# Kernel tuning notes

Hardware: AMD Instinct MI355X
Metric: run time of the kernel (lower is better)

Reference implementation:

```python
import jax, jax.numpy as jnp
import numpy as np

N_NODES = 200_000
N_UND = 3_200_000        # undirected masked edges
E = 2 * N_UND            # directed edges


def _seg_mean(m, dst, n_nodes):
    # DGL fn.mean: mean over incoming edge messages; zero-in-degree nodes get 0.
    s = jax.ops.segment_sum(m, dst, num_segments=n_nodes)
    deg = jax.ops.segment_sum(jnp.ones((m.shape[0], 1), m.dtype), dst, num_segments=n_nodes)
    return s / jnp.maximum(deg, 1.0)


def setup_inputs() -> dict:
    key = jax.random.key(0)
    ks = jax.random.split(key, 18)
    w = lambda k, s: jax.random.normal(k, s, dtype=jnp.float32) * 0.1
    return {
        'node_feat': jax.random.normal(ks[0], (N_NODES, 7), dtype=jnp.float32),
        'edge_feat': jax.random.normal(ks[1], (E, 4), dtype=jnp.float32),
        'edge_mask': jax.random.normal(ks[2], (N_UND, 1), dtype=jnp.float32),
        'src': jax.random.randint(ks[3], (E,), 0, N_NODES),
        'dst': jax.random.randint(ks[4], (E,), 0, N_NODES),
        'W1a': w(ks[5], (11, 32)), 'b1a': jnp.zeros((32,), jnp.float32),
        'W1b': w(ks[6], (32, 32)), 'b1b': jnp.zeros((32,), jnp.float32),
        'W2a': w(ks[7], (32, 32)), 'b2a': jnp.zeros((32,), jnp.float32),
        'W2b': w(ks[8], (32, 32)), 'b2b': jnp.zeros((32,), jnp.float32),
        'Wm1': w(ks[9], (32, 16)), 'bm1': jnp.zeros((16,), jnp.float32),
        'Wm2': w(ks[10], (16, 2)), 'bm2': jnp.zeros((2,), jnp.float32),
    }


def reference(node_feat, edge_feat, edge_mask, src, dst,
              W1a, b1a, W1b, b1b, W2a, b2a, W2b, b2b, Wm1, bm1, Wm2, bm2):
    n_nodes = node_feat.shape[0]
    relu = jax.nn.relu
    # interleave mask to both edge directions: [m0, m0, m1, m1, ...]
    m_full = jax.nn.sigmoid(jnp.repeat(edge_mask, 2, axis=0))  # [E, 1]
    # layer 1: masked cat(edge_h, src_h) -> mean over dst -> MLP
    msg1 = m_full * jnp.concatenate([edge_feat, node_feat[src]], axis=1)  # [E, 11]
    h = _seg_mean(msg1, dst, n_nodes)                                      # [N, 11]
    h = relu(relu(h @ W1a + b1a) @ W1b + b1b)                              # [N, 32]
    # layer 2: masked src_h -> mean over dst -> MLP
    msg2 = m_full * h[src]                                                 # [E, 32]
    h = _seg_mean(msg2, dst, n_nodes)                                      # [N, 32]
    h = relu(relu(h @ W2a + b2a) @ W2b + b2b)                              # [N, 32]
    # global max pool + readout MLP + softmax (batch_size=1 path)
    g = jnp.max(h, axis=0)                                                 # [32]
    logits = relu(g @ Wm1 + bm1) @ Wm2 + bm2                               # [2]
    return jax.nn.softmax(logits)[None, :]                                 # [1, 2]
```

## Files before the change

kernel.cpp:

```cpp
#include <hip/hip_runtime.h>
#include <hip/hip_fp16.h>
#include <math.h>

#define SCHUNK 1024
#define PMAX   80
#define BSHIFT 9
#define MAXBKT 1024
#define BINB   1024
#define EPT    8

__device__ __forceinline__ float sigmoidf_(float x) {
    return 1.0f / (1.0f + __expf(-x));
}

union I2H { int i; __half2 h; };
__device__ __forceinline__ int pack_h2(float a, float b) {
    I2H u; u.h = __floats2half2_rn(a, b); return u.i;
}
__device__ __forceinline__ float2 unpack_h2(int w) {
    I2H u; u.i = w; return __half22float2(u.h);
}

typedef int v4i_nt __attribute__((ext_vector_type(4)));
typedef float v4f_nt __attribute__((ext_vector_type(4)));
__device__ __forceinline__ int4 ldnt16(const int4* p) {
    v4i_nt v = __builtin_nontemporal_load((const v4i_nt*)p);
    return make_int4(v[0], v[1], v[2], v[3]);
}
__device__ __forceinline__ float4 ldnt16f(const float* p) {
    v4f_nt v = __builtin_nontemporal_load((const v4f_nt*)p);
    return make_float4(v[0], v[1], v[2], v[3]);
}

__global__ void hist_rank(const int* __restrict__ dst, int* __restrict__ deg,
                          int* __restrict__ rank, int E) {
    int e = blockIdx.x * blockDim.x + threadIdx.x;
    if (e < E) rank[e] = atomicAdd(&deg[dst[e]], 1);
}

__global__ void scan_part(const int* __restrict__ deg, int* __restrict__ bsum, int N) {
    __shared__ int tot[256];
    int t = threadIdx.x;
    int base = blockIdx.x * SCHUNK + t * 4;
    int s = 0;
    if (base + 3 < N) {
        int4 v = *(const int4*)(deg + base);
        s = v.x + v.y + v.z + v.w;
    } else {
#pragma unroll
        for (int j = 0; j < 4; ++j) if (base + j < N) s += deg[base + j];
    }
    tot[t] = s;
    __syncthreads();
    for (int o = 128; o >= 1; o >>= 1) {
        if (t < o) tot[t] += tot[t + o];
        __syncthreads();
    }
    if (t == 0) bsum[blockIdx.x] = tot[0];
}

__global__ void scan_mid(int* __restrict__ bsum, int* __restrict__ off, int B, int N) {
    __shared__ int tmp[256];
    int t = threadIdx.x;
    int chunk = (B + 255) / 256;
    int lo = t * chunk, hi = min(lo + chunk, B);
    int s = 0;
    for (int i = lo; i < hi; ++i) s += bsum[i];
    tmp[t] = s;
    __syncthreads();
    for (int o = 1; o < 256; o <<= 1) {
        int v = (t >= o) ? tmp[t - o] : 0;
        __syncthreads();
        tmp[t] += v;
        __syncthreads();
    }
    int run = (t == 0) ? 0 : tmp[t - 1];
    for (int i = lo; i < hi; ++i) { int d = bsum[i]; bsum[i] = run; run += d; }
    if (t == 255) off[N] = tmp[255];
}

__global__ void scan_fin(const int* __restrict__ deg, const int* __restrict__ bsum,
                         int* __restrict__ off, int N) {
    __shared__ int tots[256];
    int t = threadIdx.x;
    int base = blockIdx.x * SCHUNK + t * 4;
    int v0 = 0, v1 = 0, v2 = 0, v3 = 0;
    if (base + 3 < N) {
        int4 v = *(const int4*)(deg + base);
        v0 = v.x; v1 = v.y; v2 = v.z; v3 = v.w;
    } else {
        if (base + 0 < N) v0 = deg[base + 0];
        if (base + 1 < N) v1 = deg[base + 1];
        if (base + 2 < N) v2 = deg[base + 2];
        if (base + 3 < N) v3 = deg[base + 3];
    }
    tots[t] = v0 + v1 + v2 + v3;
    __syncthreads();
    for (int o = 1; o < 256; o <<= 1) {
        int v = (t >= o) ? tots[t - o] : 0;
        __syncthreads();
        tots[t] += v;
        __syncthreads();
    }
    int run = bsum[blockIdx.x] + ((t == 0) ? 0 : tots[t - 1]);
    if (base + 0 < N) off[base + 0] = run; run += v0;
    if (base + 1 < N) off[base + 1] = run; run += v1;
    if (base + 2 < N) off[base + 2] = run; run += v2;
    if (base + 3 < N) off[base + 3] = run;
}

__global__ void pack_nodes(const float* __restrict__ nf, int4* __restrict__ nf16, int N) {
    int n = blockIdx.x * blockDim.x + threadIdx.x;
    if (n >= N) return;
    const float* p = nf + (size_t)n * 7;
    int4 w;
    w.x = pack_h2(p[0], p[1]);
    w.y = pack_h2(p[2], p[3]);
    w.z = pack_h2(p[4], p[5]);
    w.w = pack_h2(p[6], 0.0f);
    nf16[n] = w;
}

__global__ __launch_bounds__(BINB)
void binA(const int* __restrict__ dst, const int* __restrict__ src,
          const float* __restrict__ edge_mask, const float* __restrict__ edge_feat,
          const float* __restrict__ node_feat,
          int* __restrict__ bktCnt, int4* __restrict__ region, int4* __restrict__ nf16,
          int E, int N, int nbkt, int bcap) {
    __shared__ int cnt[MAXBKT];
    __shared__ int base[MAXBKT];
    int t = threadIdx.x;
    int gt = blockIdx.x * BINB + t;
    if (gt < N) {
        const float* p = node_feat + (size_t)gt * 7;
        int4 w;
        w.x = pack_h2(p[0], p[1]);
        w.y = pack_h2(p[2], p[3]);
        w.z = pack_h2(p[4], p[5]);
        w.w = pack_h2(p[6], 0.0f);
        nf16[gt] = w;
    }
    for (int i = t; i < nbkt; i += BINB) cnt[i] = 0;
    __syncthreads();
    int4 rec[EPT];
    int  bl[EPT];
    int e0 = blockIdx.x * (BINB * EPT) + t;
#pragma unroll
    for (int j = 0; j < EPT; ++j) {
        int e = e0 + j * BINB;
        bl[j] = -1;
        if (e < E) {
            int d = dst[e];
            int s = src[e];
            float m = sigmoidf_(edge_mask[e >> 1]);
            float4 ef = ldnt16f(edge_feat + (size_t)e * 4);
            int b = d >> BSHIFT;
            int dlo = d & ((1 << BSHIFT) - 1);
            int lr = atomicAdd(&cnt[b], 1);
            rec[j].x = (dlo << 18) | s;
            rec[j].y = pack_h2(m * ef.x, m * ef.y);
            rec[j].z = pack_h2(m * ef.z, m * ef.w);
            rec[j].w = __float_as_int(m);
            bl[j] = (b << 16) | lr;
        }
    }
    __syncthreads();
    for (int i = t; i < nbkt; i += BINB)
        base[i] = atomicAdd(&bktCnt[i], cnt[i]);
    __syncthreads();
#pragma unroll
    for (int j = 0; j < EPT; ++j) {
        if (bl[j] >= 0) {
            int b = bl[j] >> 16, lr = bl[j] & 0xffff;
            int pos = base[b] + lr;
            if (pos < bcap) region[(size_t)b * bcap + pos] = rec[j];
        }
    }
}

__global__ __launch_bounds__(1024)
void fillS(const int4* __restrict__ region, const int* __restrict__ bktCnt,
           int4* __restrict__ recP, int* __restrict__ deg, int N, int bcap) {
    __shared__ int cnt[1 << BSHIFT];
    int b = blockIdx.x;
    int t = threadIdx.x;
    if (t < (1 << BSHIFT)) cnt[t] = 0;
    __syncthreads();
    int count = min(bktCnt[b], bcap);
    const int4* reg = region + (size_t)b * bcap;
    int n0 = b << BSHIFT;
    for (int i = t; i < count; i += blockDim.x) {
        int4 w = ldnt16(reg + i);
        int dlo = ((unsigned)w.x) >> 18;
        int r = atomicAdd(&cnt[dlo], 1);
        if (r < PMAX) {
            w.x &= 0x3FFFF;
            recP[(size_t)(n0 + dlo) * PMAX + r] = w;
        }
    }
    __syncthreads();
    if (t < (1 << BSHIFT) && n0 + t < N) deg[n0 + t] = cnt[t];
}

__global__ void hist_fill_p(const int* __restrict__ dst, const int* __restrict__ src,
                            const float* __restrict__ edge_mask,
                            const float* __restrict__ edge_feat,
                            const float* __restrict__ node_feat,
                            int* __restrict__ deg, int4* __restrict__ recP,
                            int4* __restrict__ nf16, int E, int N) {
    int t = blockIdx.x * blockDim.x + threadIdx.x;
    if (t < N) {
        const float* p = node_feat + (size_t)t * 7;
        int4 w;
        w.x = pack_h2(p[0], p[1]);
        w.y = pack_h2(p[2], p[3]);
        w.z = pack_h2(p[4], p[5]);
        w.w = pack_h2(p[6], 0.0f);
        nf16[t] = w;
    }
    int e0 = blockIdx.x * (blockDim.x << 2) + threadIdx.x;
    int e1 = e0 + blockDim.x;
    int e2 = e1 + blockDim.x;
    int e3 = e2 + blockDim.x;
    bool v0 = e0 < E, v1 = e1 < E, v2 = e2 < E, v3 = e3 < E;
    int d0 = 0, d1 = 0, d2 = 0, d3 = 0;
    int s0 = 0, s1 = 0, s2 = 0, s3 = 0;
    float k0 = 0, k1 = 0, k2 = 0, k3 = 0;
    float4 f0 = {}, f1 = {}, f2 = {}, f3 = {};
    if (v0) { d0 = dst[e0]; s0 = src[e0]; k0 = edge_mask[e0 >> 1]; f0 = ldnt16f(edge_feat + (size_t)e0 * 4); }
    if (v1) { d1 = dst[e1]; s1 = src[e1]; k1 = edge_mask[e1 >> 1]; f1 = ldnt16f(edge_feat + (size_t)e1 * 4); }
    if (v2) { d2 = dst[e2]; s2 = src[e2]; k2 = edge_mask[e2 >> 1]; f2 = ldnt16f(edge_feat + (size_t)e2 * 4); }
    if (v3) { d3 = dst[e3]; s3 = src[e3]; k3 = edge_mask[e3 >> 1]; f3 = ldnt16f(edge_feat + (size_t)e3 * 4); }
    float m0 = sigmoidf_(k0), m1 = sigmoidf_(k1), m2 = sigmoidf_(k2), m3 = sigmoidf_(k3);
    int4 w0, w1, w2, w3;
    w0.x = s0; w0.y = pack_h2(m0 * f0.x, m0 * f0.y); w0.z = pack_h2(m0 * f0.z, m0 * f0.w); w0.w = __float_as_int(m0);
    w1.x = s1; w1.y = pack_h2(m1 * f1.x, m1 * f1.y); w1.z = pack_h2(m1 * f1.z, m1 * f1.w); w1.w = __float_as_int(m1);
    w2.x = s2; w2.y = pack_h2(m2 * f2.x, m2 * f2.y); w2.z = pack_h2(m2 * f2.z, m2 * f2.w); w2.w = __float_as_int(m2);
    w3.x = s3; w3.y = pack_h2(m3 * f3.x, m3 * f3.y); w3.z = pack_h2(m3 * f3.z, m3 * f3.w); w3.w = __float_as_int(m3);
    int r0 = 0, r1 = 0, r2 = 0, r3 = 0;
    if (v0) r0 = atomicAdd(&deg[d0], 1);
    if (v1) r1 = atomicAdd(&deg[d1], 1);
    if (v2) r2 = atomicAdd(&deg[d2], 1);
    if (v3) r3 = atomicAdd(&deg[d3], 1);
    if (v0 && r0 < PMAX) recP[(size_t)d0 * PMAX + r0] = w0;
    if (v1 && r1 < PMAX) recP[(size_t)d1 * PMAX + r1] = w1;
    if (v2 && r2 < PMAX) recP[(size_t)d2 * PMAX + r2] = w2;
    if (v3 && r3 < PMAX) recP[(size_t)d3 * PMAX + r3] = w3;
}

__global__ void agg1_p(const int4* __restrict__ recP, const int* __restrict__ degv,
                       const int4* __restrict__ nf16,
                       const float* __restrict__ W1a, const float* __restrict__ b1a,
                       const float* __restrict__ W1b, const float* __restrict__ b1b,
                       __half* __restrict__ h1h, int N) {
    __shared__ float sW1a[11 * 32], sb1a[32], sW1b[32 * 32], sb1b[32];
    for (int i = threadIdx.x; i < 11 * 32; i += blockDim.x) sW1a[i] = W1a[i];
    for (int i = threadIdx.x; i < 32 * 32; i += blockDim.x) sW1b[i] = W1b[i];
    if (threadIdx.x < 32) { sb1a[threadIdx.x] = b1a[threadIdx.x]; sb1b[threadIdx.x] = b1b[threadIdx.x]; }
    __syncthreads();
    int n = blockIdx.x * (blockDim.x >> 2) + (threadIdx.x >> 2);
    int sub = threadIdx.x & 3;
    int deg = 0;
    size_t start = 0;
    if (n < N) { deg = degv[n]; start = (size_t)n * PMAX; }
    int dd = min(deg, PMAX);
    float x[11];
#pragma unroll
    for (int j = 0; j < 11; ++j) x[j] = 0.0f;
    int i = sub;
    for (; i + 4 < dd; i += 8) {
        int4 r0 = ldnt16(recP + start + i);
        int4 r1 = ldnt16(recP + start + i + 4);
        int4 nw0 = nf16[r0.x];
        int4 nw1 = nf16[r1.x];
        {
            float m = __int_as_float(r0.w);
            float2 e01 = unpack_h2(r0.y), e23 = unpack_h2(r0.z);
            x[0] += e01.x; x[1] += e01.y; x[2] += e23.x; x[3] += e23.y;
            float2 n01 = unpack_h2(nw0.x), n23 = unpack_h2(nw0.y);
            float2 n45 = unpack_h2(nw0.z), n6 = unpack_h2(nw0.w);
            x[4] += m * n01.x; x[5]  += m * n01.y; x[6] += m * n23.x; x[7] += m * n23.y;
            x[8] += m * n45.x; x[9]  += m * n45.y; x[10] += m * n6.x;
        }
        {
            float m = __int_as_float(r1.w);
            float2 e01 = unpack_h2(r1.y), e23 = unpack_h2(r1.z);
            x[0] += e01.x; x[1] += e01.y; x[2] += e23.x; x[3] += e23.y;
            float2 n01 = unpack_h2(nw1.x), n23 = unpack_h2(nw1.y);
            float2 n45 = unpack_h2(nw1.z), n6 = unpack_h2(nw1.w);
            x[4] += m * n01.x; x[5]  += m * n01.y; x[6] += m * n23.x; x[7] += m * n23.y;
            x[8] += m * n45.x; x[9]  += m * n45.y; x[10] += m * n6.x;
        }
    }
    for (; i < dd; i += 4) {
        int4 r = ldnt16(recP + start + i);
        float m = __int_as_float(r.w);
        float2 e01 = unpack_h2(r.y), e23 = unpack_h2(r.z);
        x[0] += e01.x; x[1] += e01.y; x[2] += e23.x; x[3] += e23.y;
        int4 nw = nf16[r.x];
        float2 n01 = unpack_h2(nw.x), n23 = unpack_h2(nw.y);
        float2 n45 = unpack_h2(nw.z), n6 = unpack_h2(nw.w);
        x[4] += m * n01.x; x[5]  += m * n01.y; x[6] += m * n23.x; x[7] += m * n23.y;
        x[8] += m * n45.x; x[9]  += m * n45.y; x[10] += m * n6.x;
    }
#pragma unroll
    for (int j = 0; j < 11; ++j) {
        x[j] += __shfl_xor(x[j], 1);
        x[j] += __shfl_xor(x[j], 2);
    }
    if (n >= N) return;
    float inv = 1.0f / fmaxf((float)deg, 1.0f);
#pragma unroll
    for (int j = 0; j < 11; ++j) x[j] *= inv;
    float hdn[32];
#pragma unroll
    for (int k = 0; k < 32; ++k) {
        float acc = sb1a[k];
#pragma unroll
        for (int j = 0; j < 11; ++j) acc += x[j] * sW1a[j * 32 + k];
        hdn[k] = fmaxf(acc, 0.0f);
    }
    float o[32];
#pragma unroll
    for (int k2 = 0; k2 < 32; ++k2) {
        float acc = sb1b[k2];
#pragma unroll
        for (int k = 0; k < 32; ++k) acc += hdn[k] * sW1b[k * 32 + k2];
        o[k2] = fmaxf(acc, 0.0f);
    }
    int4 w;
    w.x = pack_h2(o[8 * sub + 0], o[8 * sub + 1]);
    w.y = pack_h2(o[8 * sub + 2], o[8 * sub + 3]);
    w.z = pack_h2(o[8 * sub + 4], o[8 * sub + 5]);
    w.w = pack_h2(o[8 * sub + 6], o[8 * sub + 7]);
    ((int4*)(h1h + (size_t)n * 32))[sub] = w;
}

__global__ void agg2_p(const int4* __restrict__ recP, const int* __restrict__ degv,
                       const __half* __restrict__ h1h,
                       const float* __restrict__ W2a, const float* __restrict__ b2a,
                       const float* __restrict__ W2b, const float* __restrict__ b2b,
                       float* __restrict__ gmax, int N) {
    __shared__ float sW2a[32 * 32], sb2a[32], sW2b[32 * 32], sb2b[32];
    __shared__ int smax[32];
    for (int i = threadIdx.x; i < 32 * 32; i += blockDim.x) { sW2a[i] = W2a[i]; sW2b[i] = W2b[i]; }
    if (threadIdx.x < 32) {
        sb2a[threadIdx.x] = b2a[threadIdx.x];
        sb2b[threadIdx.x] = b2b[threadIdx.x];
        smax[threadIdx.x] = 0;
    }
    __syncthreads();
    int n = blockIdx.x * (blockDim.x >> 2) + (threadIdx.x >> 2);
    int sub = threadIdx.x & 3;
    bool valid = (n < N);
    int deg = 0;
    size_t start = 0;
    if (valid) { deg = degv[n]; start = (size_t)n * PMAX; }
    int dd = min(deg, PMAX);
    float x[32];
#pragma unroll
    for (int j = 0; j < 32; ++j) x[j] = 0.0f;
    int i = sub;
    for (; i + 4 < dd; i += 8) {
        int4 r0 = ldnt16(recP + start + i);
        int4 r1 = ldnt16(recP + start + i + 4);
        const int4* hp0 = (const int4*)(h1h + (size_t)r0.x * 32);
        const int4* hp1 = (const int4*)(h1h + (size_t)r1.x * 32);
        int4 g00 = hp0[0], g01 = hp0[1], g02 = hp0[2], g03 = hp0[3];
        int4 g10 = hp1[0], g11 = hp1[1], g12 = hp1[2], g13 = hp1[3];
        {
            float m = __int_as_float(r0.w);
            float2 a, b, c, d;
            a = unpack_h2(g00.x); b = unpack_h2(g00.y); c = unpack_h2(g00.z); d = unpack_h2(g00.w);
            x[0] += m * a.x; x[1] += m * a.y; x[2] += m * b.x; x[3] += m * b.y;
            x[4] += m * c.x; x[5] += m * c.y; x[6] += m * d.x; x[7] += m * d.y;
            a = unpack_h2(g01.x); b = unpack_h2(g01.y); c = unpack_h2(g01.z); d = unpack_h2(g01.w);
            x[8] += m * a.x; x[9] += m * a.y; x[10] += m * b.x; x[11] += m * b.y;
            x[12] += m * c.x; x[13] += m * c.y; x[14] += m * d.x; x[15] += m * d.y;
            a = unpack_h2(g02.x); b = unpack_h2(g02.y); c = unpack_h2(g02.z); d = unpack_h2(g02.w);
            x[16] += m * a.x; x[17] += m * a.y; x[18] += m * b.x; x[19] += m * b.y;
            x[20] += m * c.x; x[21] += m * c.y; x[22] += m * d.x; x[23] += m * d.y;
            a = unpack_h2(g03.x); b = unpack_h2(g03.y); c = unpack_h2(g03.z); d = unpack_h2(g03.w);
            x[24] += m * a.x; x[25] += m * a.y; x[26] += m * b.x; x[27] += m * b.y;
            x[28] += m * c.x; x[29] += m * c.y; x[30] += m * d.x; x[31] += m * d.y;
        }
        {
            float m = __int_as_float(r1.w);
            float2 a, b, c, d;
            a = unpack_h2(g10.x); b = unpack_h2(g10.y); c = unpack_h2(g10.z); d = unpack_h2(g10.w);
            x[0] += m * a.x; x[1] += m * a.y; x[2] += m * b.x; x[3] += m * b.y;
            x[4] += m * c.x; x[5] += m * c.y; x[6] += m * d.x; x[7] += m * d.y;
            a = unpack_h2(g11.x); b = unpack_h2(g11.y); c = unpack_h2(g11.z); d = unpack_h2(g11.w);
            x[8] += m * a.x; x[9] += m * a.y; x[10] += m * b.x; x[11] += m * b.y;
            x[12] += m * c.x; x[13] += m * c.y; x[14] += m * d.x; x[15] += m * d.y;
            a = unpack_h2(g12.x); b = unpack_h2(g12.y); c = unpack_h2(g12.z); d = unpack_h2(g12.w);
            x[16] += m * a.x; x[17] += m * a.y; x[18] += m * b.x; x[19] += m * b.y;
            x[20] += m * c.x; x[21] += m * c.y; x[22] += m * d.x; x[23] += m * d.y;
            a = unpack_h2(g13.x); b = unpack_h2(g13.y); c = unpack_h2(g13.z); d = unpack_h2(g13.w);
            x[24] += m * a.x; x[25] += m * a.y; x[26] += m * b.x; x[27] += m * b.y;
            x[28] += m * c.x; x[29] += m * c.y; x[30] += m * d.x; x[31] += m * d.y;
        }
    }
    for (; i < dd; i += 4) {
        int4 r = ldnt16(recP + start + i);
        float m = __int_as_float(r.w);
        const int4* hp = (const int4*)(h1h + (size_t)r.x * 32);
#pragma unroll
        for (int q = 0; q < 4; ++q) {
            int4 v = hp[q];
            float2 a = unpack_h2(v.x), b = unpack_h2(v.y);
            float2 c = unpack_h2(v.z), d = unpack_h2(v.w);
            x[8 * q + 0] += m * a.x; x[8 * q + 1] += m * a.y;
            x[8 * q + 2] += m * b.x; x[8 * q + 3] += m * b.y;
            x[8 * q + 4] += m * c.x; x[8 * q + 5] += m * c.y;
            x[8 * q + 6] += m * d.x; x[8 * q + 7] += m * d.y;
        }
    }
#pragma unroll
    for (int j = 0; j < 32; ++j) {
        x[j] += __shfl_xor(x[j], 1);
        x[j] += __shfl_xor(x[j], 2);
    }
    float inv = 1.0f / fmaxf((float)deg, 1.0f);
#pragma unroll
    for (int j = 0; j < 32; ++j) x[j] *= inv;
    float hdn[32];
#pragma unroll
    for (int k = 0; k < 32; ++k) {
        float acc = sb2a[k];
#pragma unroll
        for (int j = 0; j < 32; ++j) acc += x[j] * sW2a[j * 32 + k];
        hdn[k] = fmaxf(acc, 0.0f);
    }
    int lane = threadIdx.x & 63;
#pragma unroll
    for (int k2 = 0; k2 < 32; ++k2) {
        float acc = sb2b[k2];
#pragma unroll
        for (int k = 0; k < 32; ++k) acc += hdn[k] * sW2b[k * 32 + k2];
        float v = valid ? fmaxf(acc, 0.0f) : 0.0f;
#pragma unroll
        for (int o = 32; o >= 1; o >>= 1)
            v = fmaxf(v, __shfl_xor(v, o));
        if (lane == 0) atomicMax(&smax[k2], __float_as_int(v));
    }
    __syncthreads();
    if (threadIdx.x < 32) atomicMax((int*)&gmax[threadIdx.x], smax[threadIdx.x]);
}

__global__ void fill_rec16(const int* __restrict__ dst, const int* __restrict__ rank,
                           const int* __restrict__ off,
                           const float* __restrict__ edge_mask,
                           const int* __restrict__ src,
                           const float* __restrict__ edge_feat,
                           int4* __restrict__ rec, int E) {
    int e = blockIdx.x * blockDim.x + threadIdx.x;
    if (e >= E) return;
    int p = off[dst[e]] + rank[e];
    float m = sigmoidf_(edge_mask[e >> 1]);
    float4 ef = ldnt16f(edge_feat + (size_t)e * 4);
    int4 w;
    w.x = src[e];
    w.y = pack_h2(m * ef.x, m * ef.y);
    w.z = pack_h2(m * ef.z, m * ef.w);
    w.w = __float_as_int(m);
    rec[p] = w;
}

__global__ void agg1_16(const int4* __restrict__ rec, const int* __restrict__ off,
                        const int4* __restrict__ nf16,
                        const float* __restrict__ W1a, const float* __restrict__ b1a,
                        const float* __restrict__ W1b, const float* __restrict__ b1b,
                        __half* __restrict__ h1h, int N) {
    __shared__ float sW1a[11 * 32], sb1a[32], sW1b[32 * 32], sb1b[32];
    for (int i = threadIdx.x; i < 11 * 32; i += blockDim.x) sW1a[i] = W1a[i];
    for (int i = threadIdx.x; i < 32 * 32; i += blockDim.x) sW1b[i] = W1b[i];
    if (threadIdx.x < 32) { sb1a[threadIdx.x] = b1a[threadIdx.x]; sb1b[threadIdx.x] = b1b[threadIdx.x]; }
    __syncthreads();
    int n = blockIdx.x * (blockDim.x >> 2) + (threadIdx.x >> 2);
    int sub = threadIdx.x & 3;
    int start = 0, deg = 0;
    if (n < N) { start = off[n]; deg = off[n + 1] - start; }
    float x[11];
#pragma unroll
    for (int j = 0; j < 11; ++j) x[j] = 0.0f;
    for (int i = sub; i < deg; i += 4) {
        int4 r = ldnt16(rec + start + i);
        float m = __int_as_float(r.w);
        float2 e01 = unpack_h2(r.y), e23 = unpack_h2(r.z);
        x[0] += e01.x; x[1] += e01.y; x[2] += e23.x; x[3] += e23.y;
        int4 nw = nf16[r.x];
        float2 n01 = unpack_h2(nw.x), n23 = unpack_h2(nw.y);
        float2 n45 = unpack_h2(nw.z), n6 = unpack_h2(nw.w);
        x[4] += m * n01.x; x[5]  += m * n01.y; x[6] += m * n23.x; x[7] += m * n23.y;
        x[8] += m * n45.x; x[9]  += m * n45.y; x[10] += m * n6.x;
    }
#pragma unroll
    for (int j = 0; j < 11; ++j) {
        x[j] += __shfl_xor(x[j], 1);
        x[j] += __shfl_xor(x[j], 2);
    }
    if (n >= N) return;
    float inv = 1.0f / fmaxf((float)deg, 1.0f);
#pragma unroll
    for (int j = 0; j < 11; ++j) x[j] *= inv;
    float hdn[32];
#pragma unroll
    for (int k = 0; k < 32; ++k) {
        float acc = sb1a[k];
#pragma unroll
        for (int j = 0; j < 11; ++j) acc += x[j] * sW1a[j * 32 + k];
        hdn[k] = fmaxf(acc, 0.0f);
    }
    float o[32];
#pragma unroll
    for (int k2 = 0; k2 < 32; ++k2) {
        float acc = sb1b[k2];
#pragma unroll
        for (int k = 0; k < 32; ++k) acc += hdn[k] * sW1b[k * 32 + k2];
        o[k2] = fmaxf(acc, 0.0f);
    }
    int4 w;
    w.x = pack_h2(o[8 * sub + 0], o[8 * sub + 1]);
    w.y = pack_h2(o[8 * sub + 2], o[8 * sub + 3]);
    w.z = pack_h2(o[8 * sub + 4], o[8 * sub + 5]);
    w.w = pack_h2(o[8 * sub + 6], o[8 * sub + 7]);
    ((int4*)(h1h + (size_t)n * 32))[sub] = w;
}

__global__ void agg2_16(const int4* __restrict__ rec, const int* __restrict__ off,
                        const __half* __restrict__ h1h,
                        const float* __restrict__ W2a, const float* __restrict__ b2a,
                        const float* __restrict__ W2b, const float* __restrict__ b2b,
                        float* __restrict__ gmax, int N) {
    __shared__ float sW2a[32 * 32], sb2a[32], sW2b[32 * 32], sb2b[32];
    __shared__ int smax[32];
    for (int i = threadIdx.x; i < 32 * 32; i += blockDim.x) { sW2a[i] = W2a[i]; sW2b[i] = W2b[i]; }
    if (threadIdx.x < 32) {
        sb2a[threadIdx.x] = b2a[threadIdx.x];
        sb2b[threadIdx.x] = b2b[threadIdx.x];
        smax[threadIdx.x] = 0;
    }
    __syncthreads();
    int n = blockIdx.x * (blockDim.x >> 2) + (threadIdx.x >> 2);
    int sub = threadIdx.x & 3;
    bool valid = (n < N);
    int start = 0, deg = 0;
    if (valid) { start = off[n]; deg = off[n + 1] - start; }
    float x[32];
#pragma unroll
    for (int j = 0; j < 32; ++j) x[j] = 0.0f;
    for (int i = sub; i < deg; i += 4) {
        int4 r = ldnt16(rec + start + i);
        float m = __int_as_float(r.w);
        const int4* hp = (const int4*)(h1h + (size_t)r.x * 32);
#pragma unroll
        for (int q = 0; q < 4; ++q) {
            int4 v = hp[q];
            float2 a = unpack_h2(v.x), b = unpack_h2(v.y);
            float2 c = unpack_h2(v.z), d = unpack_h2(v.w);
            x[8 * q + 0] += m * a.x; x[8 * q + 1] += m * a.y;
            x[8 * q + 2] += m * b.x; x[8 * q + 3] += m * b.y;
            x[8 * q + 4] += m * c.x; x[8 * q + 5] += m * c.y;
            x[8 * q + 6] += m * d.x; x[8 * q + 7] += m * d.y;
        }
    }
#pragma unroll
    for (int j = 0; j < 32; ++j) {
        x[j] += __shfl_xor(x[j], 1);
        x[j] += __shfl_xor(x[j], 2);
    }
    float inv = 1.0f / fmaxf((float)deg, 1.0f);
#pragma unroll
    for (int j = 0; j < 32; ++j) x[j] *= inv;
    float hdn[32];
#pragma unroll
    for (int k = 0; k < 32; ++k) {
        float acc = sb2a[k];
#pragma unroll
        for (int j = 0; j < 32; ++j) acc += x[j] * sW2a[j * 32 + k];
        hdn[k] = fmaxf(acc, 0.0f);
    }
    int lane = threadIdx.x & 63;
#pragma unroll
    for (int k2 = 0; k2 < 32; ++k2) {
        float acc = sb2b[k2];
#pragma unroll
        for (int k = 0; k < 32; ++k) acc += hdn[k] * sW2b[k * 32 + k2];
        float v = valid ? fmaxf(acc, 0.0f) : 0.0f;
#pragma unroll
        for (int o = 32; o >= 1; o >>= 1)
            v = fmaxf(v, __shfl_xor(v, o));
        if (lane == 0) atomicMax(&smax[k2], __float_as_int(v));
    }
    __syncthreads();
    if (threadIdx.x < 32) atomicMax((int*)&gmax[threadIdx.x], smax[threadIdx.x]);
}

__global__ void fill_rec(const int* __restrict__ dst, const int* __restrict__ rank,
                         const int* __restrict__ off,
                         const float* __restrict__ edge_mask,
                         const int* __restrict__ src,
                         int2* __restrict__ rec, int E) {
    int e = blockIdx.x * blockDim.x + threadIdx.x;
    if (e >= E) return;
    int p = off[dst[e]] + rank[e];
    float m = sigmoidf_(edge_mask[e >> 1]);
    int mq = (int)(m * 16384.0f + 0.5f);
    mq = min(mq, 16383);
    unsigned packed = ((unsigned)src[e] << 14) | (unsigned)mq;
    rec[p] = make_int2(e, (int)packed);
}

__global__ void agg1_rec(const int2* __restrict__ rec, const int* __restrict__ off,
                         const float* __restrict__ edge_feat,
                         const float* __restrict__ node_feat,
                         const float* __restrict__ W1a, const float* __restrict__ b1a,
                         const float* __restrict__ W1b, const float* __restrict__ b1b,
                         float* __restrict__ h1, int N) {
    __shared__ float sW1a[11 * 32], sb1a[32], sW1b[32 * 32], sb1b[32];
    for (int i = threadIdx.x; i < 11 * 32; i += blockDim.x) sW1a[i] = W1a[i];
    for (int i = threadIdx.x; i < 32 * 32; i += blockDim.x) sW1b[i] = W1b[i];
    if (threadIdx.x < 32) { sb1a[threadIdx.x] = b1a[threadIdx.x]; sb1b[threadIdx.x] = b1b[threadIdx.x]; }
    __syncthreads();
    int n = blockIdx.x * blockDim.x + threadIdx.x;
    if (n >= N) return;
    int start = off[n];
    int deg = off[n + 1] - start;
    float x[11];
#pragma unroll
    for (int j = 0; j < 11; ++j) x[j] = 0.0f;
    for (int i = 0; i < deg; ++i) {
        int2 r = rec[start + i];
        int e = r.x;
        unsigned packed = (unsigned)r.y;
        int s = (int)(packed >> 14);
        float m = (float)(packed & 16383u) * (1.0f / 16384.0f);
        float4 ef = *(const float4*)(edge_feat + (size_t)e * 4);
        x[0] += m * ef.x; x[1] += m * ef.y; x[2] += m * ef.z; x[3] += m * ef.w;
        const float* nf = node_feat + (size_t)s * 7;
#pragma unroll
        for (int j = 0; j < 7; ++j) x[4 + j] += m * nf[j];
    }
    float inv = 1.0f / fmaxf((float)deg, 1.0f);
#pragma unroll
    for (int j = 0; j < 11; ++j) x[j] *= inv;
    float hdn[32];
#pragma unroll
    for (int k = 0; k < 32; ++k) {
        float acc = sb1a[k];
#pragma unroll
        for (int j = 0; j < 11; ++j) acc += x[j] * sW1a[j * 32 + k];
        hdn[k] = fmaxf(acc, 0.0f);
    }
    float o[32];
#pragma unroll
    for (int k2 = 0; k2 < 32; ++k2) {
        float acc = sb1b[k2];
#pragma unroll
        for (int k = 0; k < 32; ++k) acc += hdn[k] * sW1b[k * 32 + k2];
        o[k2] = fmaxf(acc, 0.0f);
    }
    float4* outp = (float4*)(h1 + (size_t)n * 32);
#pragma unroll
    for (int q = 0; q < 8; ++q)
        outp[q] = make_float4(o[4 * q], o[4 * q + 1], o[4 * q + 2], o[4 * q + 3]);
}

__global__ void agg2_rec(const int2* __restrict__ rec, const int* __restrict__ off,
                         const float* __restrict__ h1,
                         const float* __restrict__ W2a, const float* __restrict__ b2a,
                         const float* __restrict__ W2b, const float* __restrict__ b2b,
                         float* __restrict__ gmax, int N) {
    __shared__ float sW2a[32 * 32], sb2a[32], sW2b[32 * 32], sb2b[32];
    __shared__ int smax[32];
    for (int i = threadIdx.x; i < 32 * 32; i += blockDim.x) { sW2a[i] = W2a[i]; sW2b[i] = W2b[i]; }
    if (threadIdx.x < 32) {
        sb2a[threadIdx.x] = b2a[threadIdx.x];
        sb2b[threadIdx.x] = b2b[threadIdx.x];
        smax[threadIdx.x] = 0;
    }
    __syncthreads();
    int n = blockIdx.x * blockDim.x + threadIdx.x;
    bool valid = (n < N);
    int nn = valid ? n : 0;
    int start = valid ? off[nn] : 0;
    int deg = valid ? (off[nn + 1] - start) : 0;
    float x[32];
#pragma unroll
    for (int j = 0; j < 32; ++j) x[j] = 0.0f;
    for (int i = 0; i < deg; ++i) {
        int2 r = rec[start + i];
        unsigned packed = (unsigned)r.y;
        int s = (int)(packed >> 14);
        float m = (float)(packed & 16383u) * (1.0f / 16384.0f);
        const float4* hp = (const float4*)(h1 + (size_t)s * 32);
#pragma unroll
        for (int q = 0; q < 8; ++q) {
            float4 v = hp[q];
            x[4 * q + 0] += m * v.x;
            x[4 * q + 1] += m * v.y;
            x[4 * q + 2] += m * v.z;
            x[4 * q + 3] += m * v.w;
        }
    }
    float inv = 1.0f / fmaxf((float)deg, 1.0f);
#pragma unroll
    for (int j = 0; j < 32; ++j) x[j] *= inv;
    float hdn[32];
#pragma unroll
    for (int k = 0; k < 32; ++k) {
        float acc = sb2a[k];
#pragma unroll
        for (int j = 0; j < 32; ++j) acc += x[j] * sW2a[j * 32 + k];
        hdn[k] = fmaxf(acc, 0.0f);
    }
    int lane = threadIdx.x & 63;
#pragma unroll
    for (int k2 = 0; k2 < 32; ++k2) {
        float acc = sb2b[k2];
#pragma unroll
        for (int k = 0; k < 32; ++k) acc += hdn[k] * sW2b[k * 32 + k2];
        float v = valid ? fmaxf(acc, 0.0f) : 0.0f;
#pragma unroll
        for (int o = 32; o >= 1; o >>= 1)
            v = fmaxf(v, __shfl_xor(v, o));
        if (lane == 0) atomicMax(&smax[k2], __float_as_int(v));
    }
    __syncthreads();
    if (threadIdx.x < 32) atomicMax((int*)&gmax[threadIdx.x], smax[threadIdx.x]);
}

__global__ void readout(const float* __restrict__ gmax,
                        const float* __restrict__ Wm1, const float* __restrict__ bm1,
                        const float* __restrict__ Wm2, const float* __restrict__ bm2,
                        float* __restrict__ out) {
    __shared__ float p[16];
    int t = threadIdx.x;
    if (t < 16) {
        float acc = bm1[t];
        for (int j = 0; j < 32; ++j) acc += gmax[j] * Wm1[j * 16 + t];
        p[t] = fmaxf(acc, 0.0f);
    }
    __syncthreads();
    if (t == 0) {
        float l0 = bm2[0], l1 = bm2[1];
        for (int k = 0; k < 16; ++k) { l0 += p[k] * Wm2[k * 2]; l1 += p[k] * Wm2[k * 2 + 1]; }
        float mx = fmaxf(l0, l1);
        float e0 = __expf(l0 - mx), e1 = __expf(l1 - mx);
        float s = e0 + e1;
        out[0] = e0 / s;
        out[1] = e1 / s;
    }
}

static inline size_t align16(size_t x) { return (x + 15) & ~(size_t)15; }

extern "C" void kernel_launch(void* const* d_in, const int* in_sizes, int n_in,
                              void* d_out, int out_size, void* d_ws, size_t ws_size,
                              hipStream_t stream) {
    const float* node_feat = (const float*)d_in[0];
    const float* edge_feat = (const float*)d_in[1];
    const float* edge_mask = (const float*)d_in[2];
    const int*   src       = (const int*)d_in[3];
    const int*   dst       = (const int*)d_in[4];
    const float* W1a = (const float*)d_in[5];
    const float* b1a = (const float*)d_in[6];
    const float* W1b = (const float*)d_in[7];
    const float* b1b = (const float*)d_in[8];
    const float* W2a = (const float*)d_in[9];
    const float* b2a = (const float*)d_in[10];
    const float* W2b = (const float*)d_in[11];
    const float* b2b = (const float*)d_in[12];
    const float* Wm1 = (const float*)d_in[13];
    const float* bm1 = (const float*)d_in[14];
    const float* Wm2 = (const float*)d_in[15];
    const float* bm2 = (const float*)d_in[16];

    const int N = in_sizes[0] / 7;
    const int E = in_sizes[3];
    const int B = (N + SCHUNK - 1) / SCHUNK;

    {
        const int nbkt = (N + (1 << BSHIFT) - 1) >> BSHIFT;
        if (nbkt <= MAXBKT && N <= (1 << 18)) {
            int avg = (E + nbkt - 1) / nbkt;
            int bcap = avg + avg / 8 + 256;
            char* basep = (char*)d_ws;
            size_t off0 = 0;
            int*   bktCnt = (int*)(basep + off0);  off0 += (size_t)(nbkt + 32) * sizeof(int);
            float* gmax   = (float*)(bktCnt + nbkt);
            off0 = align16(off0);
            int*   degS   = (int*)(basep + off0);  off0 += (size_t)N * sizeof(int);
            off0 = align16(off0);
            int4*  nf16   = (int4*)(basep + off0); off0 += (size_t)N * sizeof(int4);
            int4*  recP   = (int4*)(basep + off0); off0 += (size_t)N * PMAX * sizeof(int4);
            int4*  region = (int4*)(basep + off0);
            __half* h1h   = (__half*)region;
            size_t regionBytes = (size_t)nbkt * bcap * sizeof(int4);
            size_t h1Bytes = (size_t)N * 32 * sizeof(__half);
            off0 += (regionBytes > h1Bytes ? regionBytes : h1Bytes);
            const size_t needS = off0;
            if (ws_size >= needS) {
                hipMemsetAsync(d_ws, 0, (size_t)(nbkt + 32) * sizeof(int), stream);
                const int binBlocks = (max(E, N) + BINB * EPT - 1) / (BINB * EPT);
                binA<<<binBlocks, BINB, 0, stream>>>(dst, src, edge_mask, edge_feat, node_feat,
                                                     bktCnt, region, nf16, E, N, nbkt, bcap);
                fillS<<<nbkt, 1024, 0, stream>>>(region, bktCnt, recP, degS, N, bcap);
                const int nodeBlocks = (N + 63) / 64;
                agg1_p<<<nodeBlocks, 256, 0, stream>>>(recP, degS, nf16,
                                                       W1a, b1a, W1b, b1b, h1h, N);
                agg2_p<<<nodeBlocks, 256, 0, stream>>>(recP, degS, h1h,
                                                       W2a, b2a, W2b, b2b, gmax, N);
                readout<<<1, 64, 0, stream>>>(gmax, Wm1, bm1, Wm2, bm2, (float*)d_out);
                return;
            }
        }
    }

    {
        int*    deg_i = (int*)d_ws;
        float*  gmax  = (float*)(deg_i + N);
        __half* h1h   = (__half*)(gmax + 32);
        int4*   nf16  = (int4*)(h1h + (size_t)N * 32);
        int4*   recP  = nf16 + N;
        const size_t needP = (size_t)(deg_i + N + 32 - (int*)d_ws) * sizeof(int)
                           + (size_t)N * 32 * sizeof(__half)
                           + (size_t)N * sizeof(int4)
                           + (size_t)N * PMAX * sizeof(int4);
        if (ws_size >= needP) {
            hipMemsetAsync(d_ws, 0, (size_t)(N + 32) * sizeof(int), stream);
            int threadsNeeded = max((E + 3) / 4, N);
            const int gridEF = (threadsNeeded + 255) / 256;
            hist_fill_p<<<gridEF, 256, 0, stream>>>(dst, src, edge_mask, edge_feat,
                                                    node_feat, deg_i, recP, nf16, E, N);
            const int nodeBlocks = (N + 63) / 64;
            agg1_p<<<nodeBlocks, 256, 0, stream>>>(recP, deg_i, nf16,
                                                   W1a, b1a, W1b, b1b, h1h, N);
            agg2_p<<<nodeBlocks, 256, 0, stream>>>(recP, deg_i, h1h,
                                                   W2a, b2a, W2b, b2b, gmax, N);
            readout<<<1, 64, 0, stream>>>(gmax, Wm1, bm1, Wm2, bm2, (float*)d_out);
            return;
        }
    }

    int*   deg_i = (int*)d_ws;
    float* gmax  = (float*)(deg_i + N);
    int*   off   = (int*)(gmax + 32);
    int*   bsum  = off + (N + 1);
    int*   slot  = bsum + (B + 1);

    const size_t slot16 = (size_t)E > (size_t)16 * N ? (size_t)E : (size_t)16 * N;
    int*    rank   = slot;
    __half* h1h    = (__half*)slot;
    int4*   rec16  = (int4*)(slot + slot16);
    int4*   nf16   = rec16 + E;
    const size_t need16 = ((size_t)2 * N + 34 + B + slot16 + (size_t)E * 4 + (size_t)N * 4) * sizeof(int);

    const size_t slot8 = (size_t)E > (size_t)32 * N ? (size_t)E : (size_t)32 * N;
    float* h1f  = (float*)slot;
    int2*  rec8 = (int2*)(slot + slot8);

    hipMemsetAsync(d_ws, 0, (size_t)(N + 32) * sizeof(int), stream);

    hist_rank<<<(E + 255) / 256, 256, 0, stream>>>(dst, deg_i, rank, E);
    scan_part<<<B, 256, 0, stream>>>(deg_i, bsum, N);
    scan_mid<<<1, 256, 0, stream>>>(bsum, off, B, N);
    scan_fin<<<B, 256, 0, stream>>>(deg_i, bsum, off, N);

    if (ws_size >= need16) {
        const int nodeBlocks = (N + 63) / 64;
        pack_nodes<<<(N + 255) / 256, 256, 0, stream>>>(node_feat, nf16, N);
        fill_rec16<<<(E + 255) / 256, 256, 0, stream>>>(dst, rank, off, edge_mask, src,
                                                        edge_feat, rec16, E);
        agg1_16<<<nodeBlocks, 256, 0, stream>>>(rec16, off, nf16,
                                                W1a, b1a, W1b, b1b, h1h, N);
        agg2_16<<<nodeBlocks, 256, 0, stream>>>(rec16, off, h1h,
                                                W2a, b2a, W2b, b2b, gmax, N);
    } else {
        fill_rec<<<(E + 255) / 256, 256, 0, stream>>>(dst, rank, off, edge_mask, src, rec8, E);
        agg1_rec<<<(N + 255) / 256, 256, 0, stream>>>(rec8, off, edge_feat, node_feat,
                                                      W1a, b1a, W1b, b1b, h1f, N);
        agg2_rec<<<(N + 255) / 256, 256, 0, stream>>>(rec8, off, h1f,
                                                      W2a, b2a, W2b, b2b, gmax, N);
    }
    readout<<<1, 64, 0, stream>>>(gmax, Wm1, bm1, Wm2, bm2, (float*)d_out);
}
```

Before: 668.3 us.

## Split node MLPs across 4 sub-lanes and order per-node edges by source tile

In agg1 and agg2, the four lanes that share a node no longer each compute the full 32x32 MLP redundantly. Each lane computes 8 hidden units and shares them through shuffles, so each output is computed once, and the max-pool reduction is cut to 8 values per lane. fillS gains a two-pass counting sort that groups each destination's edge records by source-index tile, which should improve locality of the later gather from node features. This adds an extra pass over the bucket region, a larger shared histogram, and more shuffles in exchange for less redundant ALU work and better cache locality.

```diff
diff --git a/kernel.cpp b/kernel.cpp
--- a/kernel.cpp
+++ b/kernel.cpp
@@ -8,6 +8,8 @@
 #define MAXBKT 1024
 #define BINB   1024
 #define EPT    8
+#define TSHIFT 15
+#define TDIM   8
 
 __device__ __forceinline__ float sigmoidf_(float x) {
     return 1.0f / (1.0f + __expf(-x));
@@ -181,25 +183,43 @@
 __global__ __launch_bounds__(1024)
 void fillS(const int4* __restrict__ region, const int* __restrict__ bktCnt,
            int4* __restrict__ recP, int* __restrict__ deg, int N, int bcap) {
-    __shared__ int cnt[1 << BSHIFT];
+    __shared__ int cnt[(1 << BSHIFT) * TDIM];
     int b = blockIdx.x;
     int t = threadIdx.x;
-    if (t < (1 << BSHIFT)) cnt[t] = 0;
+    for (int i = t; i < (1 << BSHIFT) * TDIM; i += blockDim.x) cnt[i] = 0;
     __syncthreads();
     int count = min(bktCnt[b], bcap);
     const int4* reg = region + (size_t)b * bcap;
     int n0 = b << BSHIFT;
     for (int i = t; i < count; i += blockDim.x) {
+        int wx = reg[i].x;
+        int dlo = ((unsigned)wx) >> 18;
+        int tile = (wx & 0x3FFFF) >> TSHIFT;
+        atomicAdd(&cnt[dlo * TDIM + tile], 1);
+    }
+    __syncthreads();
+    if (t < (1 << BSHIFT)) {
+        int run = 0;
+#pragma unroll
+        for (int k = 0; k < TDIM; ++k) {
+            int c = cnt[t * TDIM + k];
+            cnt[t * TDIM + k] = run;
+            run += c;
+        }
+        if (n0 + t < N) deg[n0 + t] = run;
+    }
+    __syncthreads();
+    for (int i = t; i < count; i += blockDim.x) {
         int4 w = ldnt16(reg + i);
         int dlo = ((unsigned)w.x) >> 18;
-        int r = atomicAdd(&cnt[dlo], 1);
-        if (r < PMAX) {
-            w.x &= 0x3FFFF;
-            recP[(size_t)(n0 + dlo) * PMAX + r] = w;
-        }
-    }
-    __syncthreads();
-    if (t < (1 << BSHIFT) && n0 + t < N) deg[n0 + t] = cnt[t];
+        int s = w.x & 0x3FFFF;
+        int tile = s >> TSHIFT;
+        int slot = atomicAdd(&cnt[dlo * TDIM + tile], 1);
+        if (slot < PMAX) {
+            w.x = s;
+            recP[(size_t)(n0 + dlo) * PMAX + slot] = w;
+        }
+    }
 }
 
 __global__ void hist_fill_p(const int* __restrict__ dst, const int* __restrict__ src,
@@ -312,27 +332,35 @@
     float inv = 1.0f / fmaxf((float)deg, 1.0f);
 #pragma unroll
     for (int j = 0; j < 11; ++j) x[j] *= inv;
-    float hdn[32];
-#pragma unroll
-    for (int k = 0; k < 32; ++k) {
+    float hdn8[8];
+#pragma unroll
+    for (int j = 0; j < 8; ++j) {
+        int k = sub * 8 + j;
         float acc = sb1a[k];
 #pragma unroll
-        for (int j = 0; j < 11; ++j) acc += x[j] * sW1a[j * 32 + k];
-        hdn[k] = fmaxf(acc, 0.0f);
-    }
-    float o[32];
-#pragma unroll
-    for (int k2 = 0; k2 < 32; ++k2) {
-        float acc = sb1b[k2];
-#pragma unroll
-        for (int k = 0; k < 32; ++k) acc += hdn[k] * sW1b[k * 32 + k2];
-        o[k2] = fmaxf(acc, 0.0f);
+        for (int i2 = 0; i2 < 11; ++i2) acc += x[i2] * sW1a[i2 * 32 + k];
+        hdn8[j] = fmaxf(acc, 0.0f);
+    }
+    float o8[8];
+#pragma unroll
+    for (int j = 0; j < 8; ++j) o8[j] = sb1b[sub * 8 + j];
+    int lane = threadIdx.x & 63;
+    int gb = lane & ~3;
+#pragma unroll
+    for (int g = 0; g < 4; ++g) {
+#pragma unroll
+        for (int j = 0; j < 8; ++j) {
+            float hk = __shfl(hdn8[j], gb | g, 64);
+            const float* wrow = sW1b + (g * 8 + j) * 32 + sub * 8;
+#pragma unroll
+            for (int j2 = 0; j2 < 8; ++j2) o8[j2] += hk * wrow[j2];
+        }
     }
     int4 w;
-    w.x = pack_h2(o[8 * sub + 0], o[8 * sub + 1]);
-    w.y = pack_h2(o[8 * sub + 2], o[8 * sub + 3]);
-    w.z = pack_h2(o[8 * sub + 4], o[8 * sub + 5]);
-    w.w = pack_h2(o[8 * sub + 6], o[8 * sub + 7]);
+    w.x = pack_h2(fmaxf(o8[0], 0.0f), fmaxf(o8[1], 0.0f));
+    w.y = pack_h2(fmaxf(o8[2], 0.0f), fmaxf(o8[3], 0.0f));
+    w.z = pack_h2(fmaxf(o8[4], 0.0f), fmaxf(o8[5], 0.0f));
+    w.w = pack_h2(fmaxf(o8[6], 0.0f), fmaxf(o8[7], 0.0f));
     ((int4*)(h1h + (size_t)n * 32))[sub] = w;
 }
 
@@ -424,25 +452,43 @@
     float inv = 1.0f / fmaxf((float)deg, 1.0f);
 #pragma unroll
     for (int j = 0; j < 32; ++j) x[j] *= inv;
-    float hdn[32];
-#pragma unroll
-    for (int k = 0; k < 32; ++k) {
+    float hdn8[8];
+#pragma unroll
+    for (int j = 0; j < 8; ++j) {
+        int k = sub * 8 + j;
         float acc = sb2a[k];
 #pragma unroll
-        for (int j = 0; j < 32; ++j) acc += x[j] * sW2a[j * 32 + k];
-        hdn[k] = fmaxf(acc, 0.0f);
-    }
+        for (int i2 = 0; i2 < 32; ++i2) acc += x[i2] * sW2a[i2 * 32 + k];
+        hdn8[j] = fmaxf(acc, 0.0f);
+    }
+    float o8[8];
+#pragma unroll
+    for (int j = 0; j < 8; ++j) o8[j] = sb2b[sub * 8 + j];
     int lane = threadIdx.x & 63;
-#pragma unroll
-    for (int k2 = 0; k2 < 32; ++k2) {
-        float acc = sb2b[k2];
-#pragma unroll
-        for (int k = 0; k < 32; ++k) acc += hdn[k] * sW2b[k * 32 + k2];
-        float v = valid ? fmaxf(acc, 0.0f) : 0.0f;
-#pragma unroll
-        for (int o = 32; o >= 1; o >>= 1)
-            v = fmaxf(v, __shfl_xor(v, o));
-        if (lane == 0) atomicMax(&smax[k2], __float_as_int(v));
+    int gb = lane & ~3;
+#pragma unroll
+    for (int g = 0; g < 4; ++g) {
+#pragma unroll
+        for (int j = 0; j < 8; ++j) {
+            float hk = __shfl(hdn8[j], gb | g, 64);
+            const float* wrow = sW2b + (g * 8 + j) * 32 + sub * 8;
+#pragma unroll
+            for (int j2 = 0; j2 < 8; ++j2) o8[j2] += hk * wrow[j2];
+        }
+    }
+#pragma unroll
+    for (int j2 = 0; j2 < 8; ++j2) {
+        float v = valid ? fmaxf(o8[j2], 0.0f) : 0.0f;
+        v = fmaxf(v, __shfl_xor(v, 4));
+        v = fmaxf(v, __shfl_xor(v, 8));
+        v = fmaxf(v, __shfl_xor(v, 16));
+        v = fmaxf(v, __shfl_xor(v, 32));
+        o8[j2] = v;
+    }
+    if (lane < 4) {
+#pragma unroll
+        for (int j2 = 0; j2 < 8; ++j2)
+            atomicMax(&smax[sub * 8 + j2], __float_as_int(o8[j2]));
     }
     __syncthreads();
     if (threadIdx.x < 32) atomicMax((int*)&gmax[threadIdx.x], smax[threadIdx.x]);
```

Measured after the change: 824.3 us. 1.23x slower.
